# Kernel tuning notes

Hardware: AMD Instinct MI355X
Metric: run time of the kernel (lower is better)

The kernel has to match this reference:

```python
import jax, jax.numpy as jnp
import numpy as np

EMBED = 1024
HEADS = 16
HEAD_DIM = EMBED // HEADS


def setup_inputs() -> dict:
    key = jax.random.key(0)
    ks = jax.random.split(key, 10)
    B, N, M = 4, 2048, 2048
    s = 1.0 / np.sqrt(EMBED)
    return {
        "xq": jax.random.normal(ks[0], (B, N, EMBED), jnp.float32),
        "xk": jax.random.normal(ks[1], (B, M, EMBED), jnp.float32),
        "xv": jax.random.normal(ks[2], (B, M, EMBED), jnp.float32),
        "Wq": jax.random.normal(ks[3], (EMBED, EMBED), jnp.float32) * s,
        "bq": jnp.zeros((EMBED,), jnp.float32),
        "Wk": jax.random.normal(ks[4], (EMBED, EMBED), jnp.float32) * s,
        "bk": jnp.zeros((EMBED,), jnp.float32),
        "Wv": jax.random.normal(ks[5], (EMBED, EMBED), jnp.float32) * s,
        "bv": jnp.zeros((EMBED,), jnp.float32),
        "Wo": jax.random.normal(ks[6], (EMBED, EMBED), jnp.float32) * s,
    }


def reference(xq, xk, xv, Wq, bq, Wk, bk, Wv, bv, Wo):
    B, N, _ = xq.shape
    M = xk.shape[1]
    scale = HEAD_DIM ** -0.5
    # projections -> [B, H, N/M, D]
    q = (xq @ Wq.T + bq).reshape(B, N, HEADS, HEAD_DIM).transpose(0, 2, 1, 3)
    k = (xk @ Wk.T + bk).reshape(B, M, HEADS, HEAD_DIM).transpose(0, 2, 1, 3)
    v = (xv @ Wv.T + bv).reshape(B, M, HEADS, HEAD_DIM).transpose(0, 2, 1, 3)
    scores = jnp.einsum("bhnd,bhmd->bhnm", q, k) * scale
    weights = jax.nn.softmax(scores, axis=-1)
    out = jnp.einsum("bhnm,bhmd->bhnd", weights, v)
    out = out.transpose(0, 2, 1, 3).reshape(B, N, EMBED)
    return out @ Wo.T
```

## Files before the change

kernel.cpp:

```cpp
#include <hip/hip_runtime.h>
#include <hip/hip_bf16.h>


typedef unsigned short u16;
typedef __attribute__((ext_vector_type(8))) short short8;
typedef __attribute__((ext_vector_type(4))) float f32x4;
typedef __attribute__((ext_vector_type(16))) float f32x16;
typedef __attribute__((ext_vector_type(4))) unsigned int uint4v;

__device__ __forceinline__ u16 f2bf(float f) {
  unsigned u = __float_as_uint(f);
  u = (u + 0x7FFFu + ((u >> 16) & 1u)) >> 16;
  return (u16)u;
}

__device__ __forceinline__ unsigned pack_bf2(float lo, float hi) {
  unsigned r;
  asm("v_cvt_pk_bf16_f32 %0, %1, %2" : "=v"(r) : "v"(lo), "v"(hi));
  return r;
}

#if __has_builtin(__builtin_amdgcn_exp2f)
__device__ __forceinline__ float fast_exp2(float x) { return __builtin_amdgcn_exp2f(x); }
#else
__device__ __forceinline__ float fast_exp2(float x) {
  float r;
  asm("v_exp_f32 %0, %1" : "=v"(r) : "v"(x));
  return r;
}
#endif

__device__ __forceinline__ void gload_lds16(const void* g, void* l) {
  __builtin_amdgcn_global_load_lds(
      (const __attribute__((address_space(1))) void*)g,
      (__attribute__((address_space(3))) void*)l, 16, 0, 0);
}

__device__ __forceinline__ void sbar0() { __builtin_amdgcn_sched_barrier(0); }

__global__ __launch_bounds__(256) void cvt_all(
    const float* __restrict__ xq, const float* __restrict__ xk,
    const float* __restrict__ xv, const float* __restrict__ Wq,
    const float* __restrict__ Wk, const float* __restrict__ Wv,
    const float* __restrict__ Wo,
    u16* __restrict__ oxq, u16* __restrict__ oxk, u16* __restrict__ oxv,
    u16* __restrict__ owq, u16* __restrict__ owk, u16* __restrict__ owv,
    u16* __restrict__ owo) {
  const int i = blockIdx.x * 256 + threadIdx.x;
  const float* s; u16* d; int j;
  if      (i < 2097152) { s = xq; d = oxq; j = i; }
  else if (i < 4194304) { s = xk; d = oxk; j = i - 2097152; }
  else if (i < 6291456) { s = xv; d = oxv; j = i - 4194304; }
  else if (i < 6553600) { s = Wq; d = owq; j = i - 6291456; }
  else if (i < 6815744) { s = Wk; d = owk; j = i - 6553600; }
  else if (i < 7077888) { s = Wv; d = owv; j = i - 6815744; }
  else                  { s = Wo; d = owo; j = i - 7077888; }
  const float4 v = ((const float4*)s)[j];
  uint2 u;
  u.x = pack_bf2(v.x, v.y);
  u.y = pack_bf2(v.z, v.w);
  ((uint2*)d)[j] = u;
}

template<int OUT_BF16, int BIAS_MODE>
__device__ __forceinline__ void gemm_body(
    const u16* __restrict__ A, const u16* __restrict__ Bm,
    const float* __restrict__ bias, void* __restrict__ Cout,
    int Nn, int K, float scale, int tm, int tn,
    u16 (*sA)[128 * 32], u16 (*sB)[128 * 32])
{
  const int tid = threadIdx.x;
  const int wave = tid >> 6, lane = tid & 63;
  const int row0 = tm << 7, col0 = tn << 7;
  const int lr = lane >> 2, lc8 = (lane & 3) << 3;
  const int frow = lane & 15, fk8 = (lane >> 4) << 3;
  const int wr = wave >> 1, wc = wave & 1;

  const u16* gA0 = A + (size_t)(row0 + wave * 16 + lr) * K + lc8;
  const u16* gA1 = gA0 + (size_t)64 * K;
  const u16* gB0 = Bm + (size_t)(col0 + wave * 16 + lr) * K + lc8;
  const u16* gB1 = gB0 + (size_t)64 * K;
  const int lofs = wave * 512;

  const f32x4 zf = {0.f, 0.f, 0.f, 0.f};
  f32x4 acc[4][4];
#pragma unroll
  for (int m = 0; m < 4; ++m)
#pragma unroll
    for (int n = 0; n < 4; ++n) acc[m][n] = zf;

  const int kSteps = K >> 5;
  gload_lds16(gA0, &sA[0][lofs]);
  gload_lds16(gA1, &sA[0][lofs + 2048]);
  gload_lds16(gB0, &sB[0][lofs]);
  gload_lds16(gB1, &sB[0][lofs + 2048]);
  sbar0();

  for (int kt = 0; kt < kSteps; ++kt) {
    const int cur = kt & 1;
    const int nxt = (kt + 1) & (kSteps - 1);
    const int nk0 = nxt << 5;
    gload_lds16(gA0 + nk0, &sA[cur ^ 1][lofs]);
    gload_lds16(gA1 + nk0, &sA[cur ^ 1][lofs + 2048]);
    gload_lds16(gB0 + nk0, &sB[cur ^ 1][lofs]);
    gload_lds16(gB1 + nk0, &sB[cur ^ 1][lofs + 2048]);
    sbar0();
    asm volatile("s_waitcnt vmcnt(4)" ::: "memory");
    sbar0();
    __builtin_amdgcn_s_barrier();
    sbar0();

    short8 af[4], bfr[4];
#pragma unroll
    for (int m = 0; m < 4; ++m)
      af[m] = *(const short8*)&sA[cur][(wr * 64 + m * 16 + frow) * 32 + fk8];
#pragma unroll
    for (int n = 0; n < 4; ++n)
      bfr[n] = *(const short8*)&sB[cur][(wc * 64 + n * 16 + frow) * 32 + fk8];
    __builtin_amdgcn_s_setprio(1);
#pragma unroll
    for (int m = 0; m < 4; ++m)
#pragma unroll
      for (int n = 0; n < 4; ++n)
        acc[m][n] = __builtin_amdgcn_mfma_f32_16x16x32_bf16(af[m], bfr[n], acc[m][n], 0, 0, 0);
    __builtin_amdgcn_s_setprio(0);
    sbar0();
    __builtin_amdgcn_s_barrier();
    sbar0();
  }

  const int r0 = row0 + wr * 64 + ((lane >> 4) << 2);
  const int c0 = col0 + wc * 64 + frow;
#pragma unroll
  for (int m = 0; m < 4; ++m)
#pragma unroll
    for (int n = 0; n < 4; ++n) {
      const int col = c0 + n * 16;
#pragma unroll
      for (int j = 0; j < 4; ++j) {
        float vv = acc[m][n][j];
        if (BIAS_MODE == 1) vv += bias[col];
        if (BIAS_MODE == 2) vv += bias[r0 + m * 16 + j];
        vv *= scale;
        const size_t idx = (size_t)(r0 + m * 16 + j) * Nn + col;
        if (OUT_BF16) ((u16*)Cout)[idx] = f2bf(vv);
        else          ((float*)Cout)[idx] = vv;
      }
    }
}

__global__ __launch_bounds__(256, 2) void proj3(
    const u16* __restrict__ xq, const u16* __restrict__ wq,
    const float* __restrict__ bq, u16* __restrict__ qo,
    const u16* __restrict__ xk, const u16* __restrict__ wk,
    const float* __restrict__ bk, u16* __restrict__ ko,
    const u16* __restrict__ wv, const u16* __restrict__ xv,
    const float* __restrict__ bv, u16* __restrict__ vto, float sc2)
{
  __shared__ u16 sA[2][128 * 32];
  __shared__ u16 sB[2][128 * 32];
  const int seg = blockIdx.x >> 9, idx = blockIdx.x & 511;
  const int bid2 = (idx & 7) * 64 + (idx >> 3);
  if (seg == 0)
    gemm_body<1, 1>(xq, wq, bq, qo, 1024, 1024, sc2, bid2 >> 3, bid2 & 7, sA, sB);
  else if (seg == 1)
    gemm_body<1, 1>(xk, wk, bk, ko, 1024, 1024, 1.0f, bid2 >> 3, bid2 & 7, sA, sB);
  else
    gemm_body<1, 2>(wv, xv, bv, vto, 8192, 1024, 1.0f, bid2 >> 6, bid2 & 63, sA, sB);
}

__global__ __launch_bounds__(256, 2) void gemm_wo(
    const u16* __restrict__ A, const u16* __restrict__ Bm, float* __restrict__ C)
{
  __shared__ u16 sA[2][128 * 32];
  __shared__ u16 sB[2][128 * 32];
  const int bid2 = (blockIdx.x & 7) * 64 + (blockIdx.x >> 3);
  gemm_body<0, 0>(A, Bm, nullptr, C, 1024, 1024, 1.0f, bid2 >> 3, bid2 & 7, sA, sB);
}

__global__ __launch_bounds__(256, 4) void attn_fwd(
    const u16* __restrict__ q, const u16* __restrict__ k,
    const u16* __restrict__ vt, u16* __restrict__ o)
{
  __shared__ u16 sK[2][64 * 64];
  __shared__ u16 sVt[2][64 * 64];
  const int tid = threadIdx.x, wave = tid >> 6, lane = tid & 63;
  const int l31 = lane & 31, hi = lane >> 5;
  const int bid2 = (blockIdx.x & 7) * 128 + (blockIdx.x >> 3);
  const int qt = bid2 & 15, bh = bid2 >> 4;
  const int h = bh & 15, b = bh >> 4;
  const int q0 = qt * 128 + wave * 32;
  const size_t kbase  = ((size_t)b * 2048) * 1024 + (size_t)h * 64;
  const size_t vtbase = ((size_t)h * 64) * 8192 + (size_t)b * 2048;

  const u16* qrow = q + kbase + (size_t)(q0 + l31) * 1024 + hi * 8;
  short8 qf[4];
#pragma unroll
  for (int ks = 0; ks < 4; ++ks) qf[ks] = *(const short8*)(qrow + ks * 16);

  int koff[8], voff[8];
#pragma unroll
  for (int ks = 0; ks < 4; ++ks)
#pragma unroll
    for (int kb = 0; kb < 2; ++kb) {
      const int row = kb * 32 + l31;
      koff[ks * 2 + kb] = row * 64 + ((ks * 16 + hi * 8) ^ ((row & 7) << 3));
    }
#pragma unroll
  for (int c = 0; c < 4; ++c)
#pragma unroll
    for (int nb = 0; nb < 2; ++nb) {
      const int drow = nb * 32 + l31;
      voff[c * 2 + nb] = drow * 64 + ((c * 16 + hi * 8) ^ ((drow & 7) << 3));
    }

  const int srow = tid >> 3, sch = tid & 7;
  const int swz = (sch ^ (srow & 7)) << 3;
  const u16* gK0 = k + kbase + (size_t)srow * 1024 + swz;
  const u16* gK1 = gK0 + (size_t)32 * 1024;
  const u16* gV0 = vt + vtbase + (size_t)srow * 8192 + swz;
  const u16* gV1 = gV0 + (size_t)32 * 8192;

  f32x16 ov[2] = {};
  float ll = 0.f;

  gload_lds16(gK0, &sK[0][tid * 8]);
  gload_lds16(gK1, &sK[0][tid * 8 + 2048]);
  gload_lds16(gV0, &sVt[0][tid * 8]);
  gload_lds16(gV1, &sVt[0][tid * 8 + 2048]);
  sbar0();

  for (int t = 0; t < 32; ++t) {
    const int cur = t & 1;
    {
      const int nt = (t + 1) & 31;
      const size_t nkv = (size_t)(nt << 6);
      gload_lds16(gK0 + nkv * 1024, &sK[cur ^ 1][tid * 8]);
      gload_lds16(gK1 + nkv * 1024, &sK[cur ^ 1][tid * 8 + 2048]);
      gload_lds16(gV0 + nkv, &sVt[cur ^ 1][tid * 8]);
      gload_lds16(gV1 + nkv, &sVt[cur ^ 1][tid * 8 + 2048]);
    }
    sbar0();
    asm volatile("s_waitcnt vmcnt(4)" ::: "memory");
    sbar0();
    __builtin_amdgcn_s_barrier();
    sbar0();

    const u16* bK = &sK[cur][0];
    const u16* bV = &sVt[cur][0];

    f32x16 sacc[2] = {};
    __builtin_amdgcn_s_setprio(1);
#pragma unroll
    for (int ks = 0; ks < 4; ++ks)
#pragma unroll
      for (int kb = 0; kb < 2; ++kb) {
        const short8 kf = *(const short8*)(bK + koff[ks * 2 + kb]);
        sacc[kb] = __builtin_amdgcn_mfma_f32_32x32x16_bf16(kf, qf[ks], sacc[kb], 0, 0, 0);
      }
    __builtin_amdgcn_s_setprio(0);

    float lsum = 0.f;
#pragma unroll
    for (int kb = 0; kb < 2; ++kb)
#pragma unroll
      for (int i = 0; i < 16; ++i) {
        const float p = fast_exp2(sacc[kb][i]);
        sacc[kb][i] = p;
        lsum += p;
      }
    lsum += __shfl_xor(lsum, 32);
    ll += lsum;

    __builtin_amdgcn_s_setprio(1);
#pragma unroll
    for (int c = 0; c < 4; ++c) {
      const int kb = c >> 1, rb = (c & 1) * 8;
      const unsigned A0 = pack_bf2(sacc[kb][rb + 0], sacc[kb][rb + 1]);
      const unsigned A1 = pack_bf2(sacc[kb][rb + 2], sacc[kb][rb + 3]);
      const unsigned B0 = pack_bf2(sacc[kb][rb + 4], sacc[kb][rb + 5]);
      const unsigned B1 = pack_bf2(sacc[kb][rb + 6], sacc[kb][rb + 7]);
      const auto s0 = __builtin_amdgcn_permlane32_swap(A0, B0, false, false);
      const auto s1 = __builtin_amdgcn_permlane32_swap(A1, B1, false, false);
      uint4v pw; pw[0] = s0[0]; pw[1] = s1[0]; pw[2] = s0[1]; pw[3] = s1[1];
      const short8 pa = __builtin_bit_cast(short8, pw);
#pragma unroll
      for (int nb = 0; nb < 2; ++nb) {
        const short8 vf = *(const short8*)(bV + voff[c * 2 + nb]);
        ov[nb] = __builtin_amdgcn_mfma_f32_32x32x16_bf16(pa, vf, ov[nb], 0, 0, 0);
      }
    }
    __builtin_amdgcn_s_setprio(0);
    sbar0();
    __builtin_amdgcn_s_barrier();
    sbar0();
  }

  const float inv = 1.0f / ll;
#pragma unroll
  for (int r = 0; r < 16; ++r) {
    const int qs = (r & 3) + 8 * (r >> 2) + 4 * hi;
    const float iv = __int_as_float(
        __builtin_amdgcn_ds_bpermute(qs << 2, __float_as_int(inv)));
    const size_t rowoff = kbase + (size_t)(q0 + qs) * 1024;
#pragma unroll
    for (int nb = 0; nb < 2; ++nb)
      o[rowoff + nb * 32 + l31] = f2bf(ov[nb][r] * iv);
  }
}

extern "C" void kernel_launch(void* const* d_in, const int* in_sizes, int n_in,
                              void* d_out, int out_size, void* d_ws, size_t ws_size,
                              hipStream_t stream) {
  const float* xq = (const float*)d_in[0];
  const float* xk = (const float*)d_in[1];
  const float* xv = (const float*)d_in[2];
  const float* Wq = (const float*)d_in[3];
  const float* bq = (const float*)d_in[4];
  const float* Wk = (const float*)d_in[5];
  const float* bk = (const float*)d_in[6];
  const float* Wv = (const float*)d_in[7];
  const float* bv = (const float*)d_in[8];
  const float* Wo = (const float*)d_in[9];
  float* out = (float*)d_out;

  const size_t R = 8192, E = 1024;
  u16* ws   = (u16*)d_ws;
  u16* xq_b = ws;
  u16* xk_b = ws + 1 * R * E;
  u16* xv_b = ws + 2 * R * E;
  u16* q_b  = ws + 3 * R * E;
  u16* k_b  = ws + 4 * R * E;
  u16* vt_b = ws + 5 * R * E;
  u16* wq_b = ws + 6 * R * E;
  u16* wk_b = wq_b + E * E;
  u16* wv_b = wk_b + E * E;
  u16* wo_b = wv_b + E * E;

  cvt_all<<<28672, 256, 0, stream>>>(xq, xk, xv, Wq, Wk, Wv, Wo,
                                     xq_b, xk_b, xv_b, wq_b, wk_b, wv_b, wo_b);

  const float sc2 = 0.125f * 1.44269504088896341f;
  proj3<<<1536, 256, 0, stream>>>(xq_b, wq_b, bq, q_b,
                                  xk_b, wk_b, bk, k_b,
                                  wv_b, xv_b, bv, vt_b, sc2);

  attn_fwd<<<1024, 256, 0, stream>>>(q_b, k_b, vt_b, xq_b);

  gemm_wo<<<512, 256, 0, stream>>>(xq_b, wo_b, out);
}
```

Measured before the change: 208.6 us.

## Specialize output projection GEMM with 128x64 tiles and split softmax row-sum chains

Replaces the generic gemm_body call for the output projection with a dedicated kernel that uses 128x64 tiles and 16x16x32 MFMAs, launching 1024 blocks instead of 512 for better CU coverage. In the attention kernel, the exp/row-sum loop now keeps two independent accumulators and moves the cross-half shuffle out of the loop to the end. The smaller tile lowers per-block reuse and raises global traffic for A, and the 32-wide K step per iteration means more barriers.

```diff
diff --git a/kernel.cpp b/kernel.cpp
--- a/kernel.cpp
+++ b/kernel.cpp
@@ -173,9 +173,74 @@
     const u16* __restrict__ A, const u16* __restrict__ Bm, float* __restrict__ C)
 {
   __shared__ u16 sA[2][128 * 32];
-  __shared__ u16 sB[2][128 * 32];
-  const int bid2 = (blockIdx.x & 7) * 64 + (blockIdx.x >> 3);
-  gemm_body<0, 0>(A, Bm, nullptr, C, 1024, 1024, 1.0f, bid2 >> 3, bid2 & 7, sA, sB);
+  __shared__ u16 sB[2][64 * 32];
+  const int tid = threadIdx.x;
+  const int wave = tid >> 6, lane = tid & 63;
+  const int bid2 = (blockIdx.x & 7) * 128 + (blockIdx.x >> 3);
+  const int tm = bid2 >> 4, tn = bid2 & 15;
+  const int row0 = tm << 7, col0 = tn << 6;
+  const int lr = lane >> 2, lc8 = (lane & 3) << 3;
+  const int frow = lane & 15, fk8 = (lane >> 4) << 3;
+
+  const u16* gA0 = A + (size_t)(row0 + wave * 16 + lr) * 1024 + lc8;
+  const u16* gA1 = gA0 + (size_t)64 * 1024;
+  const u16* gB0 = Bm + (size_t)(col0 + wave * 16 + lr) * 1024 + lc8;
+  const int lofs = wave * 512;
+
+  const f32x4 zf = {0.f, 0.f, 0.f, 0.f};
+  f32x4 acc[2][4];
+#pragma unroll
+  for (int m = 0; m < 2; ++m)
+#pragma unroll
+    for (int n = 0; n < 4; ++n) acc[m][n] = zf;
+
+  gload_lds16(gA0, &sA[0][lofs]);
+  gload_lds16(gA1, &sA[0][lofs + 2048]);
+  gload_lds16(gB0, &sB[0][lofs]);
+  sbar0();
+
+  for (int kt = 0; kt < 32; ++kt) {
+    const int cur = kt & 1;
+    const int nk0 = ((kt + 1) & 31) << 5;
+    gload_lds16(gA0 + nk0, &sA[cur ^ 1][lofs]);
+    gload_lds16(gA1 + nk0, &sA[cur ^ 1][lofs + 2048]);
+    gload_lds16(gB0 + nk0, &sB[cur ^ 1][lofs]);
+    sbar0();
+    asm volatile("s_waitcnt vmcnt(3)" ::: "memory");
+    sbar0();
+    __builtin_amdgcn_s_barrier();
+    sbar0();
+
+    short8 af[2], bfr[4];
+#pragma unroll
+    for (int m = 0; m < 2; ++m)
+      af[m] = *(const short8*)&sA[cur][(wave * 32 + m * 16 + frow) * 32 + fk8];
+#pragma unroll
+    for (int n = 0; n < 4; ++n)
+      bfr[n] = *(const short8*)&sB[cur][(n * 16 + frow) * 32 + fk8];
+    __builtin_amdgcn_s_setprio(1);
+#pragma unroll
+    for (int m = 0; m < 2; ++m)
+#pragma unroll
+      for (int n = 0; n < 4; ++n)
+        acc[m][n] = __builtin_amdgcn_mfma_f32_16x16x32_bf16(af[m], bfr[n], acc[m][n], 0, 0, 0);
+    __builtin_amdgcn_s_setprio(0);
+    sbar0();
+    __builtin_amdgcn_s_barrier();
+    sbar0();
+  }
+
+  const int r0 = row0 + wave * 32 + ((lane >> 4) << 2);
+  const int c0 = col0 + frow;
+#pragma unroll
+  for (int m = 0; m < 2; ++m)
+#pragma unroll
+    for (int n = 0; n < 4; ++n) {
+      const int col = c0 + n * 16;
+#pragma unroll
+      for (int j = 0; j < 4; ++j)
+        C[(size_t)(r0 + m * 16 + j) * 1024 + col] = acc[m][n][j];
+    }
 }
 
 __global__ __launch_bounds__(256, 4) void attn_fwd(
@@ -222,7 +287,7 @@
   const u16* gV1 = gV0 + (size_t)32 * 8192;
 
   f32x16 ov[2] = {};
-  float ll = 0.f;
+  float lx = 0.f, ly = 0.f;
 
   gload_lds16(gK0, &sK[0][tid * 8]);
   gload_lds16(gK1, &sK[0][tid * 8 + 2048]);
@@ -260,17 +325,15 @@
       }
     __builtin_amdgcn_s_setprio(0);
 
-    float lsum = 0.f;
-#pragma unroll
-    for (int kb = 0; kb < 2; ++kb)
-#pragma unroll
-      for (int i = 0; i < 16; ++i) {
-        const float p = fast_exp2(sacc[kb][i]);
-        sacc[kb][i] = p;
-        lsum += p;
-      }
-    lsum += __shfl_xor(lsum, 32);
-    ll += lsum;
+    float la = 0.f, lb = 0.f;
+#pragma unroll
+    for (int i = 0; i < 16; ++i) {
+      const float p0 = fast_exp2(sacc[0][i]);
+      const float p1 = fast_exp2(sacc[1][i]);
+      sacc[0][i] = p0; la += p0;
+      sacc[1][i] = p1; lb += p1;
+    }
+    lx += la; ly += lb;
 
     __builtin_amdgcn_s_setprio(1);
 #pragma unroll
@@ -296,6 +359,8 @@
     sbar0();
   }
 
+  float ll = lx + ly;
+  ll += __shfl_xor(ll, 32);
   const float inv = 1.0f / ll;
 #pragma unroll
   for (int r = 0; r < 16; ++r) {
@@ -347,5 +412,5 @@
 
   attn_fwd<<<1024, 256, 0, stream>>>(q_b, k_b, vt_b, xq_b);
 
-  gemm_wo<<<512, 256, 0, stream>>>(xq_b, wo_b, out);
-}
+  gemm_wo<<<1024, 256, 0, stream>>>(xq_b, wo_b, out);
+}
```

Result: slower. 214.0 us (+2.6%).
